# Kernel tuning notes

Measured on AMD Instinct MI355X. Metric: run time of the kernel, lower is better.

## Reference

```python
import jax, jax.numpy as jnp
import numpy as np
import math

B, SEQ_IN, D_IN = 4, 1028, 64
D = 1024          # hidden_size
H = 16            # num_heads
HD = D // H       # head_dim
L = 4             # num_layers
D_OUT = 1
EPS = 1e-6


def setup_inputs() -> dict:
    key = jax.random.key(0)
    ks = iter(jax.random.split(key, 32))
    s = 0.02
    inp = {}
    inp['x'] = jax.random.normal(next(ks), (B, SEQ_IN, D_IN), jnp.float32)
    # conv frontend (torch Conv1d weight layout: [out_ch, in_ch, k])
    inp['conv1_w'] = jax.random.normal(next(ks), (D // 2, D_IN, 3), jnp.float32) * s
    inp['conv1_b'] = jnp.zeros((D // 2,), jnp.float32)
    inp['conv2_w'] = jax.random.normal(next(ks), (D, D // 2, 3), jnp.float32) * s
    inp['conv2_b'] = jnp.zeros((D,), jnp.float32)
    # stacked per-layer params [L, ...]
    inp['lnA_w'] = jnp.ones((L, D), jnp.float32)
    inp['lnA_b'] = jnp.zeros((L, D), jnp.float32)
    inp['q_w'] = jax.random.normal(next(ks), (L, D, D), jnp.float32) * s
    inp['q_b'] = jnp.zeros((L, D), jnp.float32)
    inp['k_w'] = jax.random.normal(next(ks), (L, D, D), jnp.float32) * s
    inp['k_b'] = jnp.zeros((L, D), jnp.float32)
    inp['v_w'] = jax.random.normal(next(ks), (L, D, D), jnp.float32) * s
    inp['v_b'] = jnp.zeros((L, D), jnp.float32)
    inp['o_w'] = jax.random.normal(next(ks), (L, D, D), jnp.float32) * s
    inp['o_b'] = jnp.zeros((L, D), jnp.float32)
    inp['lnB_w'] = jnp.ones((L, D), jnp.float32)
    inp['lnB_b'] = jnp.zeros((L, D), jnp.float32)
    inp['f1_w'] = jax.random.normal(next(ks), (L, 2 * D, D), jnp.float32) * s
    inp['f1_b'] = jnp.zeros((L, 2 * D), jnp.float32)
    inp['f2_w'] = jax.random.normal(next(ks), (L, D, 2 * D), jnp.float32) * s
    inp['f2_b'] = jnp.zeros((L, D), jnp.float32)
    inp['fc_w'] = jax.random.normal(next(ks), (D_OUT, D), jnp.float32) * s
    inp['fc_b'] = jnp.zeros((D_OUT,), jnp.float32)
    return inp


def _layernorm(x, w, b):
    # torch-style: unbiased std (ddof=1), eps added to std (not var)
    mean = jnp.mean(x, axis=-1, keepdims=True)
    var = jnp.sum((x - mean) ** 2, axis=-1, keepdims=True) / (x.shape[-1] - 1)
    return w * ((x - mean) / (jnp.sqrt(var) + EPS)) + b


def _pos_encoding(S, d):
    pos = jnp.arange(S, dtype=jnp.float32)[:, None]
    div = jnp.exp(jnp.arange(0, d, 2, dtype=jnp.float32) * (-math.log(10000.0) / d))
    pe = jnp.zeros((S, d), jnp.float32)
    pe = pe.at[:, 0::2].set(jnp.sin(pos * div))
    pe = pe.at[:, 1::2].set(jnp.cos(pos * div))
    return pe


def _forward(x, conv1_w, conv1_b, conv2_w, conv2_b,
             lnA_w, lnA_b, q_w, q_b, k_w, k_b, v_w, v_b, o_w, o_b,
             lnB_w, lnB_b, f1_w, f1_b, f2_w, f2_b, fc_w, fc_b):
    dn = ('NCH', 'OIH', 'NCH')
    h = jnp.transpose(x, (0, 2, 1))                       # [B, D_in, S_in]
    h = jax.lax.conv_general_dilated(h, conv1_w, (1,), 'VALID', dimension_numbers=dn) + conv1_b[None, :, None]
    h = jax.lax.conv_general_dilated(h, conv2_w, (1,), 'VALID', dimension_numbers=dn) + conv2_b[None, :, None]
    h = jnp.transpose(h, (0, 2, 1))                       # [B, S, D]
    S = h.shape[1]
    h = h + _pos_encoding(S, D)[None]
    scale = 1.0 / math.sqrt(HD)

    def layer(xc, p):
        (lnaw, lnab, qw, qb, kw, kb, vw, vb, ow, ob,
         lnbw, lnbb, f1w, f1b, f2w, f2b) = p
        hn = _layernorm(xc, lnaw, lnab)
        q = (hn @ qw.T + qb).reshape(B, S, H, HD).transpose(0, 2, 1, 3)
        k = (hn @ kw.T + kb).reshape(B, S, H, HD).transpose(0, 2, 1, 3)
        v = (hn @ vw.T + vb).reshape(B, S, H, HD).transpose(0, 2, 1, 3)
        scores = jnp.einsum('bhsd,bhtd->bhst', q, k) * scale
        attn = scores / (1.0 + jnp.abs(scores))           # softsign, NOT softmax
        wv = jnp.einsum('bhst,bhtd->bhsd', attn, v)
        wv = wv.transpose(0, 2, 1, 3).reshape(B, S, D)
        xc = xc + (wv @ ow.T + ob)
        hn2 = _layernorm(xc, lnbw, lnbb)
        ff = jax.nn.relu(hn2 @ f1w.T + f1b) @ f2w.T + f2b
        return xc + ff, None

    params = (lnA_w, lnA_b, q_w, q_b, k_w, k_b, v_w, v_b, o_w, o_b,
              lnB_w, lnB_b, f1_w, f1_b, f2_w, f2_b)
    h, _ = jax.lax.scan(layer, h, params)
    pooled = jnp.mean(h, axis=1)                          # [B, D]
    return pooled @ fc_w.T + fc_b                         # [B, D_OUT]


def reference(x, conv1_w, conv1_b, conv2_w, conv2_b,
              lnA_w, lnA_b, q_w, q_b, k_w, k_b, v_w, v_b, o_w, o_b,
              lnB_w, lnB_b, f1_w, f1_b, f2_w, f2_b, fc_w, fc_b):
    return _forward(x, conv1_w, conv1_b, conv2_w, conv2_b,
                    lnA_w, lnA_b, q_w, q_b, k_w, k_b, v_w, v_b, o_w, o_b,
                    lnB_w, lnB_b, f1_w, f1_b, f2_w, f2_b, fc_w, fc_b)
```

## Files before the change

### kernel.cpp

```cpp
#include <hip/hip_runtime.h>
#include <hip/hip_bf16.h>
#include <math.h>

typedef __bf16 v8bf __attribute__((ext_vector_type(8)));
typedef float  v4f  __attribute__((ext_vector_type(4)));
typedef unsigned short v8us __attribute__((ext_vector_type(8)));

__device__ __forceinline__ unsigned short f2bfu(float f) {
    unsigned u = __builtin_bit_cast(unsigned, f);
    unsigned r = (u + 0x7fffu + ((u >> 16) & 1u)) >> 16;
    return (unsigned short)r;
}
__device__ __forceinline__ float bf2f(unsigned short u) {
    unsigned x = ((unsigned)u) << 16;
    return __builtin_bit_cast(float, x);
}

__device__ __forceinline__ long long swidx(int r, int k, int kt ) {
    return ((long long)((r >> 4) * kt + (k >> 5)) << 9)
         + (((k >> 3) & 3) << 7) + ((r & 15) << 3) + (k & 7);
}

#define GLDS16(g, s)                                                        \
    __builtin_amdgcn_global_load_lds(                                       \
        (const __attribute__((address_space(1))) void*)(g),                 \
        (__attribute__((address_space(3))) void*)(s), 16, 0, 0)

#define LOAD_CHUNK(R, C) do {                                               \
    const long long o_ = (long long)(C) << 9;                               \
    _Pragma("unroll")                                                       \
    for (int i_ = 0; i_ < 4; i_++) Ab[R][i_] = *(const v8bf*)(pa[i_] + o_); \
    _Pragma("unroll")                                                       \
    for (int j_ = 0; j_ < 4; j_++) Bb[R][j_] = *(const v8bf*)(pb[j_] + o_); \
} while (0)

#define MFMA_CHUNK(R) do {                                                  \
    _Pragma("unroll")                                                       \
    for (int i_ = 0; i_ < 4; i_++)                                          \
    _Pragma("unroll")                                                       \
    for (int j_ = 0; j_ < 4; j_++)                                          \
        acc[i_][j_] = __builtin_amdgcn_mfma_f32_16x16x32_bf16(              \
            Ab[R][i_], Bb[R][j_], acc[i_][j_], 0, 0, 0);                    \
} while (0)

__global__ __launch_bounds__(64, 2) void gemm_sw_k(
    const unsigned short* __restrict__ Asw,
    const unsigned short* __restrict__ Bsw,
    const float* __restrict__ bias,
    const float* __restrict__ res,
    float* __restrict__ Cf,
    unsigned short* __restrict__ Cb,
    unsigned short* __restrict__ Csw,
    unsigned short* __restrict__ Ct, int ctcol0,
    int M, int N, int K, int ldC, int relu)
{
    const int l = threadIdx.x;

    int bx = blockIdx.x, by = blockIdx.y;
    {
        int nbx = gridDim.x;
        int nb  = nbx * gridDim.y;
        if ((nb & 7) == 0) {
            int bid = by * nbx + bx;
            int nid = (bid & 7) * (nb >> 3) + (bid >> 3);
            by = nid / nbx;
            bx = nid - by * nbx;
        }
    }
    const int m0 = by * 64;
    const int n0 = bx * 64;
    const int r16 = l & 15;
    const int qb  = l >> 4;
    const int kt = K >> 5;

    const unsigned short* pa[4];
#pragma unroll
    for (int i = 0; i < 4; i++)
        pa[i] = Asw + ((long long)(((m0 >> 4) + i) * kt) << 9) + l * 8;
    const unsigned short* pb[4];
#pragma unroll
    for (int j = 0; j < 4; j++)
        pb[j] = Bsw + ((long long)(((n0 >> 4) + j) * kt) << 9) + l * 8;

    v4f acc[4][4];
#pragma unroll
    for (int i = 0; i < 4; i++)
#pragma unroll
        for (int j = 0; j < 4; j++) acc[i][j] = (v4f){0.f, 0.f, 0.f, 0.f};

    v8bf Ab[4][4], Bb[4][4];

    LOAD_CHUNK(0, 0);
    LOAD_CHUNK(1, 1);
    LOAD_CHUNK(2, 2);

    int s = 0;
    for (; s < kt - 4; s += 4) {
        LOAD_CHUNK(3, s + 3); MFMA_CHUNK(0);
        LOAD_CHUNK(0, s + 4); MFMA_CHUNK(1);
        LOAD_CHUNK(1, s + 5); MFMA_CHUNK(2);
        LOAD_CHUNK(2, s + 6); MFMA_CHUNK(3);
    }
    LOAD_CHUNK(3, kt - 1);
    MFMA_CHUNK(0); MFMA_CHUNK(1); MFMA_CHUNK(2); MFMA_CHUNK(3);

    float bv[4];
#pragma unroll
    for (int j = 0; j < 4; j++) bv[j] = bias[n0 + 16 * j + r16];
    const int colbase = n0 + r16;
    const int nt = N >> 5;
#pragma unroll
    for (int i = 0; i < 4; i++) {
        int rowb = m0 + 16 * i + qb * 4;
#pragma unroll
        for (int j = 0; j < 4; j++) {
            int col = colbase + 16 * j;
            float v[4];
#pragma unroll
            for (int r = 0; r < 4; r++) v[r] = acc[i][j][r] + bv[j];
            if (Ct && col >= ctcol0) {
                ushort4 o;
                o.x = f2bfu(v[0]); o.y = f2bfu(v[1]);
                o.z = f2bfu(v[2]); o.w = f2bfu(v[3]);
                *(ushort4*)(Ct + ((long long)(rowb >> 10) << 20)
                            + (long long)(col - ctcol0) * 1024 + (rowb & 1023)) = o;
            } else if (Csw) {
#pragma unroll
                for (int r = 0; r < 4; r++) {
                    int row = rowb + r;
                    float vv = v[r];
                    if (relu) vv = fmaxf(vv, 0.f);
                    Csw[swidx(row, col, nt)] = f2bfu(vv);
                }
            } else {
#pragma unroll
                for (int r = 0; r < 4; r++) {
                    int row = rowb + r;
                    long long off = (long long)row * ldC + col;
                    float vv = v[r];
                    if (res)  vv += res[off];
                    if (relu) vv = fmaxf(vv, 0.f);
                    if (Cf) Cf[off] = vv;
                    if (Cb) ((unsigned short*)Cb)[off] = f2bfu(vv);
                }
            }
        }
    }
}

__global__ __launch_bounds__(256) void gemm_mfma_k(
    const __hip_bfloat16* __restrict__ A, int rpbA, long long bstrideA, int ldA,
    const __hip_bfloat16* __restrict__ B,
    const float* __restrict__ bias,
    const float* __restrict__ res,
    float* __restrict__ Cf,
    __hip_bfloat16* __restrict__ Cb,
    int M, int N, int K, int ldC, int relu)
{
    __shared__ __align__(16) __hip_bfloat16 As[2][8][64][8];
    __shared__ __align__(16) __hip_bfloat16 Bs[2][4][64][8];
    const int t  = threadIdx.x;
    const int w  = t >> 6;
    const int l  = t & 63;
    const int m0 = blockIdx.y * 128;
    const int n0 = blockIdx.x * 64;
    const int r16 = l & 15;
    const int qb  = l >> 4;
    const int wm = w >> 1, wn = w & 1;

    const __hip_bfloat16* gA[2];
#pragma unroll
    for (int tt = 0; tt < 2; tt++) {
        int arow = m0 + 16 * (2 * w + tt) + r16;
        gA[tt] = A + (long long)(arow / rpbA) * bstrideA
                   + (long long)(arow % rpbA) * ldA + qb * 8;
    }
    const __hip_bfloat16* gB = B + (long long)(n0 + 16 * w + r16) * K + qb * 8;

    v4f acc[4][2];
#pragma unroll
    for (int i = 0; i < 4; i++)
#pragma unroll
        for (int j = 0; j < 2; j++) acc[i][j] = (v4f){0.f, 0.f, 0.f, 0.f};

    GLDS16(gA[0], &As[0][2 * w + 0][0][0]);
    GLDS16(gA[1], &As[0][2 * w + 1][0][0]);
    GLDS16(gB,    &Bs[0][w][0][0]);
    __syncthreads();

    int cur = 0;
    for (int k0 = 32; k0 < K; k0 += 32) {
        v8bf af[4], bfr[2];
#pragma unroll
        for (int i = 0; i < 4; i++) af[i]  = *(const v8bf*)(&As[cur][4 * wm + i][l][0]);
#pragma unroll
        for (int j = 0; j < 2; j++) bfr[j] = *(const v8bf*)(&Bs[cur][2 * wn + j][l][0]);
        GLDS16(gA[0] + k0, &As[cur ^ 1][2 * w + 0][0][0]);
        GLDS16(gA[1] + k0, &As[cur ^ 1][2 * w + 1][0][0]);
        GLDS16(gB + k0,    &Bs[cur ^ 1][w][0][0]);
#pragma unroll
        for (int i = 0; i < 4; i++)
#pragma unroll
            for (int j = 0; j < 2; j++)
                acc[i][j] = __builtin_amdgcn_mfma_f32_16x16x32_bf16(
                    af[i], bfr[j], acc[i][j], 0, 0, 0);
        __syncthreads();
        cur ^= 1;
    }
    {
        v8bf af[4], bfr[2];
#pragma unroll
        for (int i = 0; i < 4; i++) af[i]  = *(const v8bf*)(&As[cur][4 * wm + i][l][0]);
#pragma unroll
        for (int j = 0; j < 2; j++) bfr[j] = *(const v8bf*)(&Bs[cur][2 * wn + j][l][0]);
#pragma unroll
        for (int i = 0; i < 4; i++)
#pragma unroll
            for (int j = 0; j < 2; j++)
                acc[i][j] = __builtin_amdgcn_mfma_f32_16x16x32_bf16(
                    af[i], bfr[j], acc[i][j], 0, 0, 0);
    }

    float bv[2];
#pragma unroll
    for (int j = 0; j < 2; j++) bv[j] = bias[n0 + 32 * wn + 16 * j + r16];
    const int colbase = n0 + 32 * wn + r16;
#pragma unroll
    for (int i = 0; i < 4; i++) {
        int rowb = m0 + 64 * wm + 16 * i + qb * 4;
#pragma unroll
        for (int j = 0; j < 2; j++) {
            int col = colbase + 16 * j;
#pragma unroll
            for (int r = 0; r < 4; r++) {
                int row = rowb + r;
                if (row >= M) continue;
                long long off = (long long)row * ldC + col;
                float vv = acc[i][j][r] + bv[j];
                if (res)  vv += res[off];
                if (relu) vv = fmaxf(vv, 0.f);
                if (Cf) Cf[off] = vv;
                if (Cb) ((unsigned short*)Cb)[off] = f2bfu(vv);
            }
        }
    }
}

__global__ __launch_bounds__(256) void attn_mfma_k(
    const unsigned short* __restrict__ QKV,
    const unsigned short* __restrict__ Vt,
    unsigned short* __restrict__ Osw)
{
    __shared__ __align__(16) unsigned short lds[25600];
    const int t = threadIdx.x, w = t >> 6, l = t & 63;
    const int bh = blockIdx.y, b = bh >> 4, h = bh & 15;
    const int s0 = blockIdx.x << 7;
    const int r16 = l & 15, q4 = l >> 4;
    const long long qrow0 = (long long)(b << 10) + s0;
    const int hoff = h << 6;

#pragma unroll
    for (int mi = 0; mi < 2; mi++)
#pragma unroll
        for (int kk = 0; kk < 2; kk++) {
            const unsigned short* g = QKV + (qrow0 + 32 * w + 16 * mi + r16) * 3072
                                      + hoff + 32 * kk + q4 * 8;
            GLDS16(g, &lds[(w * 4 + mi * 2 + kk) * 512]);
        }
    __syncthreads();
    v8bf qf[2][2];
#pragma unroll
    for (int mi = 0; mi < 2; mi++)
#pragma unroll
        for (int kk = 0; kk < 2; kk++)
            qf[mi][kk] = *(const v8bf*)&lds[(w * 4 + mi * 2 + kk) * 512 + l * 8];

    v4f oacc[2][4];
#pragma unroll
    for (int i = 0; i < 2; i++)
#pragma unroll
        for (int j = 0; j < 4; j++) oacc[i][j] = (v4f){0.f, 0.f, 0.f, 0.f};

    for (int t0 = 0; t0 < 1024; t0 += 64) {
#pragma unroll
        for (int rr = 0; rr < 2; rr++) {
            int r = 2 * w + rr, kk = r >> 2, j = r & 3;
            const unsigned short* gk = QKV
                + ((long long)(b << 10) + t0 + 16 * j + r16) * 3072
                + 1024 + hoff + 32 * kk + q4 * 8;
            GLDS16(gk, &lds[8192 + r * 512]);
            const unsigned short* gv = Vt + ((long long)b << 20)
                + (long long)(hoff + 16 * j + r16) * 1024 + t0 + 32 * kk + q4 * 8;
            GLDS16(gv, &lds[12288 + r * 512]);
        }
        __syncthreads();

        v8bf kf[2][4];
#pragma unroll
        for (int kk = 0; kk < 2; kk++)
#pragma unroll
            for (int j = 0; j < 4; j++)
                kf[kk][j] = *(const v8bf*)&lds[8192 + (kk * 4 + j) * 512 + l * 8];
        v4f sc[2][4];
#pragma unroll
        for (int i = 0; i < 2; i++)
#pragma unroll
            for (int j = 0; j < 4; j++) sc[i][j] = (v4f){0.f, 0.f, 0.f, 0.f};
#pragma unroll
        for (int kk = 0; kk < 2; kk++)
#pragma unroll
            for (int mi = 0; mi < 2; mi++)
#pragma unroll
                for (int j = 0; j < 4; j++)
                    sc[mi][j] = __builtin_amdgcn_mfma_f32_16x16x32_bf16(
                        qf[mi][kk], kf[kk][j], sc[mi][j], 0, 0, 0);

#pragma unroll
        for (int mi = 0; mi < 2; mi++)
#pragma unroll
            for (int j = 0; j < 4; j++)
#pragma unroll
                for (int r = 0; r < 4; r++) {
                    float v = sc[mi][j][r] * 0.125f;
                    float p = v * __builtin_amdgcn_rcpf(1.0f + fabsf(v));
                    lds[16384 + (32 * w + 16 * mi + q4 * 4 + r) * 72 + 16 * j + r16] = f2bfu(p);
                }

        v8bf pf[2][2], vf[2][4];
#pragma unroll
        for (int mi = 0; mi < 2; mi++)
#pragma unroll
            for (int kk = 0; kk < 2; kk++)
                pf[mi][kk] = *(const v8bf*)&lds[16384 + (32 * w + 16 * mi + r16) * 72
                                                + 32 * kk + q4 * 8];
#pragma unroll
        for (int kk = 0; kk < 2; kk++)
#pragma unroll
            for (int j = 0; j < 4; j++)
                vf[kk][j] = *(const v8bf*)&lds[12288 + (kk * 4 + j) * 512 + l * 8];
#pragma unroll
        for (int kk = 0; kk < 2; kk++)
#pragma unroll
            for (int mi = 0; mi < 2; mi++)
#pragma unroll
                for (int j = 0; j < 4; j++)
                    oacc[mi][j] = __builtin_amdgcn_mfma_f32_16x16x32_bf16(
                        pf[mi][kk], vf[kk][j], oacc[mi][j], 0, 0, 0);
        __syncthreads();
    }

#pragma unroll
    for (int mi = 0; mi < 2; mi++)
#pragma unroll
        for (int j = 0; j < 4; j++)
#pragma unroll
            for (int r = 0; r < 4; r++)
                lds[(32 * w + 16 * mi + q4 * 4 + r) * 72 + 16 * j + r16] =
                    f2bfu(oacc[mi][j][r]);
    __syncthreads();
    {
        int row = t >> 1, ch = (t & 1) << 5;
        int grow = (int)qrow0 + row;
#pragma unroll
        for (int i = 0; i < 4; i++) {
            int c0 = hoff + ch + 8 * i;
            v8us vv = *(const v8us*)&lds[row * 72 + ch + 8 * i];
            *(v8us*)(Osw + swidx(grow, c0, 32)) = vv;
        }
    }
}

__global__ __launch_bounds__(256) void layernorm_k(
    const float* __restrict__ x, const float* __restrict__ w,
    const float* __restrict__ b, unsigned short* __restrict__ ysw)
{
    int row = blockIdx.x;
    int t = threadIdx.x;
    float4 v = ((const float4*)(x + ((long long)row << 10)))[t];
    float s = v.x + v.y + v.z + v.w;
#pragma unroll
    for (int o = 32; o; o >>= 1) s += __shfl_down(s, o);
    __shared__ float red[4];
    __shared__ float red2[4];
    int wid = t >> 6, lane = t & 63;
    if (lane == 0) red[wid] = s;
    __syncthreads();
    float mean = (red[0] + red[1] + red[2] + red[3]) * (1.0f / 1024.0f);
    float dx = v.x - mean, dy = v.y - mean, dz = v.z - mean, dw = v.w - mean;
    float sq = dx * dx + dy * dy + dz * dz + dw * dw;
#pragma unroll
    for (int o = 32; o; o >>= 1) sq += __shfl_down(sq, o);
    if (lane == 0) red2[wid] = sq;
    __syncthreads();
    float var = (red2[0] + red2[1] + red2[2] + red2[3]) * (1.0f / 1023.0f);
    float inv = 1.0f / (sqrtf(var) + 1e-6f);
    float4 W  = ((const float4*)w)[t];
    float4 Bv = ((const float4*)b)[t];
    ushort4 o;
    o.x = f2bfu(W.x * (dx * inv) + Bv.x);
    o.y = f2bfu(W.y * (dy * inv) + Bv.y);
    o.z = f2bfu(W.z * (dz * inv) + Bv.z);
    o.w = f2bfu(W.w * (dw * inv) + Bv.w);
    int c0 = t << 2;
    *(ushort4*)(ysw + swidx(row, c0, 32)) = o;
}

__global__ __launch_bounds__(256) void add_pos_k(float* __restrict__ h)
{
    int idx = blockIdx.x * 256 + threadIdx.x;
    int d = idx & 1023;
    int s = (idx >> 10) & 1023;
    int e = d & ~1;
    float div = expf(-9.210340371976184f * (float)e * (1.0f / 1024.0f));
    float arg = (float)s * div;
    float pe = (d & 1) ? cosf(arg) : sinf(arg);
    h[idx] += pe;
}

__global__ __launch_bounds__(256) void convert_k(
    const float* __restrict__ src, unsigned short* __restrict__ dst, int n4)
{
    int i = blockIdx.x * 256 + threadIdx.x;
    if (i >= n4) return;
    float4 v = ((const float4*)src)[i];
    ushort4 o;
    o.x = f2bfu(v.x); o.y = f2bfu(v.y); o.z = f2bfu(v.z); o.w = f2bfu(v.w);
    ((ushort4*)dst)[i] = o;
}

__global__ __launch_bounds__(256) void convert_layer_sw_k(
    const float* __restrict__ q, const float* __restrict__ k,
    const float* __restrict__ v, const float* __restrict__ o,
    const float* __restrict__ f1, const float* __restrict__ f2,
    unsigned short* __restrict__ dst)
{
    int idx = blockIdx.x * 256 + threadIdx.x;
    const float* src;
    unsigned short* db;
    int Ksh, rf;
    if (idx < 0x100000) {
        int region = idx >> 18;
        rf = idx & 0x3FFFF;
        src = (region == 0) ? q : (region == 1) ? k : (region == 2) ? v : o;
        db = dst + ((long long)region << 20);
        Ksh = 10;
    } else if (idx < 0x180000) {
        rf = idx - 0x100000; src = f1; db = dst + (4LL << 20); Ksh = 10;
    } else {
        rf = idx - 0x180000; src = f2; db = dst + (6LL << 20); Ksh = 11;
    }
    float4 vv = ((const float4*)src)[rf];
    int flatf = rf << 2;
    int n  = flatf >> Ksh;
    int k0 = flatf & ((1 << Ksh) - 1);
    ushort4 ov;
    ov.x = f2bfu(vv.x); ov.y = f2bfu(vv.y); ov.z = f2bfu(vv.z); ov.w = f2bfu(vv.w);
    *(ushort4*)(db + swidx(n, k0, 1 << (Ksh - 5))) = ov;
}

__global__ __launch_bounds__(256) void concat3_k(
    const float* __restrict__ a, const float* __restrict__ b,
    const float* __restrict__ c, float* __restrict__ o)
{
    int i = blockIdx.x * 256 + threadIdx.x;
    o[i] = (i < 1024) ? a[i] : ((i < 2048) ? b[i - 1024] : c[i - 2048]);
}

__global__ __launch_bounds__(256) void reorder_w_k(
    const float* __restrict__ src, unsigned short* __restrict__ dst, int OC, int IC)
{
    int idx = blockIdx.x * 256 + threadIdx.x;
    if (idx >= OC * IC * 3) return;
    int k  = idx % 3;
    int ic = (idx / 3) % IC;
    int oc = idx / (3 * IC);
    dst[(oc * 3 + k) * IC + ic] = f2bfu(src[idx]);
}

__global__ __launch_bounds__(256) void meanpool_part_k(
    const float* __restrict__ h, float* __restrict__ part)
{
    int g = blockIdx.x;
    int b = g >> 6, rblk = g & 63;
    const float4* base = (const float4*)(h + ((long long)b << 20)
                                           + ((long long)(rblk * 16) << 10));
    float4 s = {0.f, 0.f, 0.f, 0.f};
#pragma unroll
    for (int i = 0; i < 16; i++) {
        float4 v = base[i * 256 + threadIdx.x];
        s.x += v.x; s.y += v.y; s.z += v.z; s.w += v.w;
    }
    ((float4*)part)[g * 256 + threadIdx.x] = s;
}

__global__ __launch_bounds__(256) void meanpool_red_k(
    const float* __restrict__ part, float* __restrict__ pooled)
{
    int idx = blockIdx.x * 256 + threadIdx.x;
    int b = idx >> 10, d = idx & 1023;
    const float* p = part + ((long long)(b * 64) << 10) + d;
    float s = 0.f;
#pragma unroll 8
    for (int r = 0; r < 64; r++) s += p[r << 10];
    pooled[idx] = s * (1.0f / 1024.0f);
}

__global__ __launch_bounds__(256) void fc_k(
    const float* __restrict__ p, const float* __restrict__ w,
    const float* __restrict__ fb, float* __restrict__ out)
{
    int b = blockIdx.x, t = threadIdx.x;
    float s = 0.f;
    for (int i = t; i < 1024; i += 256) s += p[(b << 10) + i] * w[i];
#pragma unroll
    for (int o = 32; o; o >>= 1) s += __shfl_down(s, o);
    __shared__ float red[4];
    if ((t & 63) == 0) red[t >> 6] = s;
    __syncthreads();
    if (t == 0) out[b] = red[0] + red[1] + red[2] + red[3] + fb[0];
}

extern "C" void kernel_launch(void* const* d_in, const int* in_sizes, int n_in,
                              void* d_out, int out_size, void* d_ws, size_t ws_size,
                              hipStream_t stream)
{
    const float* x    = (const float*)d_in[0];
    const float* c1w  = (const float*)d_in[1];
    const float* c1b  = (const float*)d_in[2];
    const float* c2w  = (const float*)d_in[3];
    const float* c2b  = (const float*)d_in[4];
    const float* lnAw = (const float*)d_in[5];
    const float* lnAb = (const float*)d_in[6];
    const float* qw   = (const float*)d_in[7];
    const float* qbi  = (const float*)d_in[8];
    const float* kw   = (const float*)d_in[9];
    const float* kbi  = (const float*)d_in[10];
    const float* vw   = (const float*)d_in[11];
    const float* vbi  = (const float*)d_in[12];
    const float* ow   = (const float*)d_in[13];
    const float* obi  = (const float*)d_in[14];
    const float* lnBw = (const float*)d_in[15];
    const float* lnBb = (const float*)d_in[16];
    const float* f1w  = (const float*)d_in[17];
    const float* f1b  = (const float*)d_in[18];
    const float* f2w  = (const float*)d_in[19];
    const float* f2b  = (const float*)d_in[20];
    const float* fcw  = (const float*)d_in[21];
    const float* fcb  = (const float*)d_in[22];
    float* out = (float*)d_out;

    float* ws = (float*)d_ws;
    typedef __hip_bfloat16 bf;
    typedef unsigned short us;
    float* h    = ws;
    us* hn_b    = (us*)(ws + 4194304);
    us* qkv_b   = (us*)(ws + 6291456);
    us* ff_b    = qkv_b;
    us* wq_b    = (us*)(ws + 12582912);
    us* wo_b    = (us*)(ws + 14155776);
    us* wf1_b   = (us*)(ws + 14680064);
    us* wf2_b   = (us*)(ws + 15728640);
    us* xb      = (us*)(ws + 16777216);
    us* h1b     = (us*)(ws + 16912896);
    us* w1t_b   = (us*)(ws + 17963520);
    us* w2t_b   = (us*)(ws + 18012672);
    float* pooled = ws + 18799104;
    us* Vt      = (us*)(ws + 18803200);
    float* bqkv = ws + 20900352;
    float* mp_part = ws + 20903424;

    convert_k<<<dim3(257), 256, 0, stream>>>(x, xb, 65792);
    reorder_w_k<<<dim3(384),  256, 0, stream>>>(c1w, w1t_b, 512, 64);
    reorder_w_k<<<dim3(6144), 256, 0, stream>>>(c2w, w2t_b, 1024, 512);

    gemm_mfma_k<<<dim3(8, 33), 256, 0, stream>>>(
        (const bf*)xb, 1026, 1028LL * 64, 64, (const bf*)w1t_b,
        c1b, nullptr, nullptr, (bf*)h1b, 4104, 512, 192, 512, 0);
    gemm_mfma_k<<<dim3(16, 32), 256, 0, stream>>>(
        (const bf*)h1b, 1024, 1026LL * 512, 512, (const bf*)w2t_b,
        c2b, nullptr, h, nullptr, 4096, 1024, 1536, 1024, 0);
    add_pos_k<<<dim3(16384), 256, 0, stream>>>(h);

    for (int l = 0; l < 4; l++) {
        long long wo  = (long long)l * 1048576;
        long long wo2 = (long long)l * 2097152;
        convert_layer_sw_k<<<dim3(8192), 256, 0, stream>>>(
            qw + wo, kw + wo, vw + wo, ow + wo, f1w + wo2, f2w + wo2, wq_b);
        concat3_k<<<dim3(12), 256, 0, stream>>>(qbi + l * 1024, kbi + l * 1024,
                                                vbi + l * 1024, bqkv);

        layernorm_k<<<dim3(4096), 256, 0, stream>>>(h, lnAw + l * 1024, lnAb + l * 1024, hn_b);
        gemm_sw_k<<<dim3(48, 64), 64, 0, stream>>>(
            hn_b, wq_b, bqkv, nullptr, nullptr, qkv_b, nullptr, Vt, 2048,
            4096, 3072, 1024, 3072, 0);
        attn_mfma_k<<<dim3(8, 64), 256, 0, stream>>>(qkv_b, Vt, hn_b);
        gemm_sw_k<<<dim3(16, 64), 64, 0, stream>>>(
            hn_b, wo_b, obi + l * 1024, h, h, nullptr, nullptr, nullptr, 0,
            4096, 1024, 1024, 1024, 0);
        layernorm_k<<<dim3(4096), 256, 0, stream>>>(h, lnBw + l * 1024, lnBb + l * 1024, hn_b);
        gemm_sw_k<<<dim3(32, 64), 64, 0, stream>>>(
            hn_b, wf1_b, f1b + l * 2048, nullptr, nullptr, nullptr, ff_b, nullptr, 0,
            4096, 2048, 1024, 2048, 1);
        gemm_sw_k<<<dim3(16, 64), 64, 0, stream>>>(
            ff_b, wf2_b, f2b + l * 1024, h, h, nullptr, nullptr, nullptr, 0,
            4096, 1024, 2048, 1024, 0);
    }

    meanpool_part_k<<<dim3(256), 256, 0, stream>>>(h, mp_part);
    meanpool_red_k<<<dim3(16), 256, 0, stream>>>(mp_part, pooled);
    fc_k<<<dim3(4), 256, 0, stream>>>(pooled, fcw, fcb, out);
}
```

Baseline: 1.143 ms.

## Widen swizzled GEMM tile to 64x128 and drop register prefetch pipeline

The single-wave swizzled GEMM now computes a 64x128 output tile instead of 64x64, doubling the accumulators per wave and halving the grid width of all four per-layer GEMM launches. The explicit 4-stage register prefetch of A/B chunks is replaced by a simple per-k loop that loads and immediately issues MFMAs. This raises arithmetic intensity per A load, but removes software latency hiding and increases register pressure, which may lower occupancy under launch_bounds(64,2).

Result: slower. 1.644 ms (+43.8%).

```diff
diff --git a/kernel.cpp b/kernel.cpp
--- a/kernel.cpp
+++ b/kernel.cpp
@@ -25,23 +25,6 @@
     __builtin_amdgcn_global_load_lds(                                       \
         (const __attribute__((address_space(1))) void*)(g),                 \
         (__attribute__((address_space(3))) void*)(s), 16, 0, 0)
-
-#define LOAD_CHUNK(R, C) do {                                               \
-    const long long o_ = (long long)(C) << 9;                               \
-    _Pragma("unroll")                                                       \
-    for (int i_ = 0; i_ < 4; i_++) Ab[R][i_] = *(const v8bf*)(pa[i_] + o_); \
-    _Pragma("unroll")                                                       \
-    for (int j_ = 0; j_ < 4; j_++) Bb[R][j_] = *(const v8bf*)(pb[j_] + o_); \
-} while (0)
-
-#define MFMA_CHUNK(R) do {                                                  \
-    _Pragma("unroll")                                                       \
-    for (int i_ = 0; i_ < 4; i_++)                                          \
-    _Pragma("unroll")                                                       \
-    for (int j_ = 0; j_ < 4; j_++)                                          \
-        acc[i_][j_] = __builtin_amdgcn_mfma_f32_16x16x32_bf16(              \
-            Ab[R][i_], Bb[R][j_], acc[i_][j_], 0, 0, 0);                    \
-} while (0)
 
 __global__ __launch_bounds__(64, 2) void gemm_sw_k(
     const unsigned short* __restrict__ Asw,
@@ -68,7 +51,7 @@
         }
     }
     const int m0 = by * 64;
-    const int n0 = bx * 64;
+    const int n0 = bx * 128;
     const int r16 = l & 15;
     const int qb  = l >> 4;
     const int kt = K >> 5;
@@ -77,43 +60,42 @@
 #pragma unroll
     for (int i = 0; i < 4; i++)
         pa[i] = Asw + ((long long)(((m0 >> 4) + i) * kt) << 9) + l * 8;
-    const unsigned short* pb[4];
-#pragma unroll
-    for (int j = 0; j < 4; j++)
+    const unsigned short* pb[8];
+#pragma unroll
+    for (int j = 0; j < 8; j++)
         pb[j] = Bsw + ((long long)(((n0 >> 4) + j) * kt) << 9) + l * 8;
 
-    v4f acc[4][4];
+    v4f acc[4][8];
 #pragma unroll
     for (int i = 0; i < 4; i++)
 #pragma unroll
-        for (int j = 0; j < 4; j++) acc[i][j] = (v4f){0.f, 0.f, 0.f, 0.f};
-
-    v8bf Ab[4][4], Bb[4][4];
-
-    LOAD_CHUNK(0, 0);
-    LOAD_CHUNK(1, 1);
-    LOAD_CHUNK(2, 2);
-
-    int s = 0;
-    for (; s < kt - 4; s += 4) {
-        LOAD_CHUNK(3, s + 3); MFMA_CHUNK(0);
-        LOAD_CHUNK(0, s + 4); MFMA_CHUNK(1);
-        LOAD_CHUNK(1, s + 5); MFMA_CHUNK(2);
-        LOAD_CHUNK(2, s + 6); MFMA_CHUNK(3);
-    }
-    LOAD_CHUNK(3, kt - 1);
-    MFMA_CHUNK(0); MFMA_CHUNK(1); MFMA_CHUNK(2); MFMA_CHUNK(3);
-
-    float bv[4];
-#pragma unroll
-    for (int j = 0; j < 4; j++) bv[j] = bias[n0 + 16 * j + r16];
+        for (int j = 0; j < 8; j++) acc[i][j] = (v4f){0.f, 0.f, 0.f, 0.f};
+
+    for (int c = 0; c < kt; ++c) {
+        const long long o = (long long)c << 9;
+        v8bf av[4], bfv[8];
+#pragma unroll
+        for (int i = 0; i < 4; i++) av[i] = *(const v8bf*)(pa[i] + o);
+#pragma unroll
+        for (int j = 0; j < 8; j++) bfv[j] = *(const v8bf*)(pb[j] + o);
+#pragma unroll
+        for (int i = 0; i < 4; i++)
+#pragma unroll
+            for (int j = 0; j < 8; j++)
+                acc[i][j] = __builtin_amdgcn_mfma_f32_16x16x32_bf16(
+                    av[i], bfv[j], acc[i][j], 0, 0, 0);
+    }
+
+    float bv[8];
+#pragma unroll
+    for (int j = 0; j < 8; j++) bv[j] = bias[n0 + 16 * j + r16];
     const int colbase = n0 + r16;
     const int nt = N >> 5;
 #pragma unroll
     for (int i = 0; i < 4; i++) {
         int rowb = m0 + 16 * i + qb * 4;
 #pragma unroll
-        for (int j = 0; j < 4; j++) {
+        for (int j = 0; j < 8; j++) {
             int col = colbase + 16 * j;
             float v[4];
 #pragma unroll
@@ -590,18 +572,18 @@
                                                 vbi + l * 1024, bqkv);
 
         layernorm_k<<<dim3(4096), 256, 0, stream>>>(h, lnAw + l * 1024, lnAb + l * 1024, hn_b);
-        gemm_sw_k<<<dim3(48, 64), 64, 0, stream>>>(
+        gemm_sw_k<<<dim3(24, 64), 64, 0, stream>>>(
             hn_b, wq_b, bqkv, nullptr, nullptr, qkv_b, nullptr, Vt, 2048,
             4096, 3072, 1024, 3072, 0);
         attn_mfma_k<<<dim3(8, 64), 256, 0, stream>>>(qkv_b, Vt, hn_b);
-        gemm_sw_k<<<dim3(16, 64), 64, 0, stream>>>(
+        gemm_sw_k<<<dim3(8, 64), 64, 0, stream>>>(
             hn_b, wo_b, obi + l * 1024, h, h, nullptr, nullptr, nullptr, 0,
             4096, 1024, 1024, 1024, 0);
         layernorm_k<<<dim3(4096), 256, 0, stream>>>(h, lnBw + l * 1024, lnBb + l * 1024, hn_b);
-        gemm_sw_k<<<dim3(32, 64), 64, 0, stream>>>(
+        gemm_sw_k<<<dim3(16, 64), 64, 0, stream>>>(
             hn_b, wf1_b, f1b + l * 2048, nullptr, nullptr, nullptr, ff_b, nullptr, 0,
             4096, 2048, 1024, 2048, 1);
-        gemm_sw_k<<<dim3(16, 64), 64, 0, stream>>>(
+        gemm_sw_k<<<dim3(8, 64), 64, 0, stream>>>(
             ff_b, wf2_b, f2b + l * 1024, h, h, nullptr, nullptr, nullptr, 0,
             4096, 1024, 2048, 1024, 0);
     }
```
